# Optimization experiments

Measured on AMD Instinct MI355X. Metric: run time of the kernel, lower is better.

## Reference

```python
import jax, jax.numpy as jnp
import numpy as np
import math

B, C, H, W = 4, 256, 64, 64
G = 32  # norm_groups
EPS = 1e-5


def conv1x1(x, w, b=None):
    # x: [B,C,H,W], w: [O,C] (squeezed 1x1 kernel)
    y = jnp.einsum('bchw,oc->bohw', x, w)
    if b is not None:
        y = y + b[None, :, None, None]
    return y


def group_norm(x, gamma, beta):
    b, c, h, w = x.shape
    xg = x.reshape(b, G, c // G, h, w)
    mu = xg.mean(axis=(2, 3, 4), keepdims=True)
    var = xg.var(axis=(2, 3, 4), keepdims=True)
    xg = (xg - mu) * jax.lax.rsqrt(var + EPS)
    x = xg.reshape(b, c, h, w)
    return x * gamma[None, :, None, None] + beta[None, :, None, None]


def setup_inputs() -> dict:
    key = jax.random.key(0)
    ks = jax.random.split(key, 12)
    s = 0.02
    return {
        'x1': jax.random.normal(ks[0], (B, C, H, W), jnp.float32),
        'x2': jax.random.normal(ks[1], (B, C, H, W), jnp.float32),
        'w1': jax.random.normal(ks[2], (C, C), jnp.float32) * s,
        'b1': jnp.zeros((C,), jnp.float32),
        'w2': jax.random.normal(ks[3], (C, C), jnp.float32) * s,
        'b2': jnp.zeros((C,), jnp.float32),
        'gn_w': jnp.ones((C,), jnp.float32),
        'gn_b': jnp.zeros((C,), jnp.float32),
        'wqkv': jax.random.normal(ks[4], (3 * C, C), jnp.float32) * s,
        'wout': jax.random.normal(ks[5], (C, C), jnp.float32) * s,
        'bout': jnp.zeros((C,), jnp.float32),
        'wsk': jax.random.normal(ks[6], (C, C), jnp.float32) * s,
        'bsk': jnp.zeros((C,), jnp.float32),
    }


def reference(x1, x2, w1, b1, w2, b2, gn_w, gn_b, wqkv, wout, bout, wsk, bsk):
    x1 = conv1x1(x1, w1, b1)
    x2 = conv1x1(x2, w2, b2)

    qkv1 = conv1x1(group_norm(x1, gn_w, gn_b), wqkv)  # [B,3C,H,W]
    qkv2 = conv1x1(group_norm(x2, gn_w, gn_b), wqkv)
    q1 = qkv1[:, :C].reshape(B, C, H * W)
    k2 = qkv2[:, C:2 * C].reshape(B, C, H * W)
    v2 = qkv2[:, 2 * C:].reshape(B, C, H * W)

    # full spatial attention: [B, HW, HW]
    attn = jnp.einsum('bcq,bck->bqk', q1, k2) / math.sqrt(C)
    attn = jax.nn.softmax(attn, axis=-1)
    out = jnp.einsum('bqk,bck->bcq', attn, v2).reshape(B, C, H, W)

    out = conv1x1(out, wout, bout)
    return out + conv1x1(x1, wsk, bsk)
```

## Files before the change

kernel.cpp:

```cpp
#include <hip/hip_runtime.h>

typedef unsigned int uint;
typedef unsigned short ushort;
typedef __bf16 bf16x8 __attribute__((ext_vector_type(8)));
typedef short s16x4 __attribute__((ext_vector_type(4)));
typedef float f32x4 __attribute__((ext_vector_type(4)));

__device__ __forceinline__ ushort f2bf(float f) {
  union { float f; uint u; } c; c.f = f;
  uint u = c.u + 0x7fffu + ((c.u >> 16) & 1u);
  return (ushort)(u >> 16);
}
__device__ __forceinline__ float bflo(uint u) { union { uint u; float f; } c; c.u = u << 16; return c.f; }
__device__ __forceinline__ float bfhi(uint u) { union { uint u; float f; } c; c.u = u & 0xffff0000u; return c.f; }

__device__ __forceinline__ void gload16(const void* g, void* l) {
  __builtin_amdgcn_global_load_lds((const __attribute__((address_space(1))) void*)g,
                                   (__attribute__((address_space(3))) void*)l, 16, 0, 0);
}
__device__ __forceinline__ void mfma16(f32x4& acc, s16x4 a, s16x4 b) {
  asm("v_mfma_f32_16x16x16_bf16 %0, %1, %2, %0" : "+v"(acc) : "v"(a), "v"(b));
}
__device__ __forceinline__ float fexp2(float x) {
  float y; asm("v_exp_f32 %0, %1" : "=v"(y) : "v"(x)); return y;
}

__global__ void cast_all(const float* __restrict__ x1, const float* __restrict__ x2,
                         const float* __restrict__ w1, const float* __restrict__ w2,
                         const float* __restrict__ wqkv, const float* __restrict__ wout,
                         const float* __restrict__ wsk,
                         ushort* __restrict__ x1t, ushort* __restrict__ x2t,
                         ushort* __restrict__ w1b, ushort* __restrict__ w2b,
                         ushort* __restrict__ wqb, ushort* __restrict__ wkvb,
                         ushort* __restrict__ woutb, ushort* __restrict__ wskb) {
  const int bid = blockIdx.x, tid = threadIdx.x;
  if (bid < 8192) {
    __shared__ float t[32][33];
    const int pc = bid & 127, cc = (bid >> 7) & 7, z = bid >> 10;
    const int b = z & 3, tn = z >> 2;
    const float* x = tn ? x2 : x1;
    ushort* xt = tn ? x2t : x1t;
    const int tx = tid & 31, ty = tid >> 5;
    const float* xb = x + ((size_t)b * 256 + cc * 32) * 4096 + pc * 32;
#pragma unroll
    for (int i = 0; i < 4; ++i)
      t[ty * 4 + i][tx] = xb[(size_t)(ty * 4 + i) * 4096 + tx];
    __syncthreads();
    ushort* xtb = xt + ((size_t)b * 4096 + pc * 32) * 256 + cc * 32;
#pragma unroll
    for (int i = 0; i < 4; ++i)
      xtb[(size_t)(ty * 4 + i) * 256 + tx] = f2bf(t[tx][ty * 4 + i]);
  } else {
    const int i = (bid - 8192) * 256 + tid;
    const float QS = 0.0625f * 1.44269504088896f;
    if (i < 65536) w1b[i] = f2bf(w1[i]);
    else if (i < 131072) w2b[i - 65536] = f2bf(w2[i - 65536]);
    else if (i < 196608) wqb[i - 131072] = f2bf(wqkv[i - 131072] * QS);
    else if (i < 327680) wkvb[i - 196608] = f2bf(wqkv[i - 131072]);
    else if (i < 393216) woutb[i - 327680] = f2bf(wout[i - 327680]);
    else wskb[i - 393216] = f2bf(wsk[i - 393216]);
  }
}

__device__ __forceinline__ void g_stage_a64(const ushort* __restrict__ A,
                                            int m0, int ko, ushort* al, int w, int l) {
#pragma unroll
  for (int j = 0; j < 2; ++j) {
    int cb = (j * 4 + w) * 64;
    int chunk = cb + l;
    int row = chunk >> 3, sl = chunk & 7;
    int col = (sl * 8) ^ ((row & 7) << 3);
    gload16(A + (size_t)(m0 + row) * 256 + ko + col, al + chunk * 8);
  }
}

__device__ __forceinline__ void g_stage_b64(const ushort* __restrict__ W,
                                            int n0, int ko, ushort* bl, int w, int l) {
#pragma unroll
  for (int j = 0; j < 4; ++j) {
    int cb = (j * 4 + w) * 64;
    int chunk = cb + l;
    int row = chunk >> 3, sl = chunk & 7;
    int col = (sl * 8) ^ ((row & 7) << 3);
    gload16(W + (size_t)(n0 + row) * 256 + ko + col, bl + chunk * 8);
  }
}

__device__ __forceinline__ void g_compute64(const ushort* al, const ushort* bl,
                                            int w, int lr, int lg, f32x4 acc[4][2]) {
#pragma unroll
  for (int kk = 0; kk < 2; ++kk) {
    bf16x8 af[4], bfr[2];
#pragma unroll
    for (int m = 0; m < 4; ++m)
      af[m] = *(const bf16x8*)&al[(m * 16 + lr) * 64 + ((kk * 32 + lg * 8) ^ ((lr & 7) << 3))];
#pragma unroll
    for (int n = 0; n < 2; ++n)
      bfr[n] = *(const bf16x8*)&bl[(w * 32 + n * 16 + lr) * 64 + ((kk * 32 + lg * 8) ^ ((lr & 7) << 3))];
#pragma unroll
    for (int m = 0; m < 4; ++m)
#pragma unroll
      for (int n = 0; n < 2; ++n)
        acc[m][n] = __builtin_amdgcn_mfma_f32_16x16x32_bf16(af[m], bfr[n], acc[m][n], 0, 0, 0);
  }
}

__launch_bounds__(256)
__global__ void conv_pair(const ushort* __restrict__ x1t, const ushort* __restrict__ x2t,
                          const ushort* __restrict__ w1b, const ushort* __restrict__ w2b,
                          const float* __restrict__ b1, const float* __restrict__ b2,
                          ushort* __restrict__ y1t, ushort* __restrict__ y2t,
                          float* __restrict__ pbuf) {
  __shared__ ushort al[2][4096];
  __shared__ ushort bl[2][8192];
  const int z = blockIdx.z, b = z & 3, t = z >> 2;
  const ushort* A = (t ? x2t : x1t) + (size_t)b * 4096 * 256;
  const ushort* W = t ? w2b : w1b;
  const float* bias = t ? b2 : b1;
  ushort* out = t ? y2t : y1t;
  const int m0 = blockIdx.y * 64, n0 = blockIdx.x * 128;
  const int tid = threadIdx.x, w = tid >> 6, l = tid & 63;
  const int lr = l & 15, lg = l >> 4;
  f32x4 acc[4][2] = {};
  g_stage_a64(A, m0, 0, al[0], w, l);
  g_stage_b64(W, n0, 0, bl[0], w, l);
  __syncthreads();
  for (int s = 0; s < 4; ++s) {
    int cur = s & 1;
    if (s + 1 < 4) {
      g_stage_a64(A, m0, (s + 1) * 64, al[cur ^ 1], w, l);
      g_stage_b64(W, n0, (s + 1) * 64, bl[cur ^ 1], w, l);
    }
    g_compute64(al[cur], bl[cur], w, lr, lg, acc);
    __syncthreads();
  }
  float sg[2] = { 0.f, 0.f }, sq[2] = { 0.f, 0.f };
#pragma unroll
  for (int n = 0; n < 2; ++n) {
    int o = n0 + w * 32 + n * 16 + lr;
    float bv = bias[o];
#pragma unroll
    for (int m = 0; m < 4; ++m) {
      int p0 = m0 + m * 16 + lg * 4;
#pragma unroll
      for (int r = 0; r < 4; ++r) {
        float val = acc[m][n][r] + bv;
        out[((size_t)b * 4096 + p0 + r) * 256 + o] = f2bf(val);
        sg[n] += val; sq[n] += val * val;
      }
    }
  }
#pragma unroll
  for (int n = 0; n < 2; ++n) {
    float s1 = sg[n], s2 = sq[n];
    s1 += __shfl_xor(s1, 16); s2 += __shfl_xor(s2, 16);
    s1 += __shfl_xor(s1, 32); s2 += __shfl_xor(s2, 32);
    s1 += __shfl_xor(s1, 1);  s2 += __shfl_xor(s2, 1);
    s1 += __shfl_xor(s1, 2);  s2 += __shfl_xor(s2, 2);
    s1 += __shfl_xor(s1, 4);  s2 += __shfl_xor(s2, 4);
    if (l == 0 || l == 8) {
      int go = (n0 + w * 32 + n * 16 + (l & 8)) >> 3;
      float* dst = pbuf + (size_t)((((t * 4 + b) * 32 + go) * 64) + blockIdx.y) * 2;
      dst[0] = s1; dst[1] = s2;
    }
  }
}

__launch_bounds__(256)
__global__ void gemm_qkv(const ushort* __restrict__ y1t, const ushort* __restrict__ y2t,
                         const ushort* __restrict__ wqb, const ushort* __restrict__ wkvb,
                         const float* __restrict__ pbuf, const float* __restrict__ gn_w,
                         const float* __restrict__ gn_b,
                         ushort* __restrict__ q1t, ushort* __restrict__ k2t, ushort* __restrict__ v2) {
  __shared__ ushort al[2][4096];
  __shared__ ushort bl[2][8192];
  __shared__ float tabs[512];
  const int b = blockIdx.z, x = blockIdx.x;
  const bool isq = x < 2;
  const ushort* A = (isq ? y1t : y2t) + (size_t)b * 4096 * 256;
  const ushort* W = isq ? wqb : wkvb;
  const int n0 = isq ? x * 128 : (x - 2) * 128;
  const int m0 = blockIdx.y * 64;
  const int tid = threadIdx.x, w = tid >> 6, l = tid & 63;
  const int lr = l & 15, lg = l >> 4;

  g_stage_b64(W, n0, 0, bl[0], w, l);

  {
    const int t = isq ? 0 : 1, c = tid, g = c >> 3;
    const float* p = pbuf + (size_t)(((t * 4 + b) * 32 + g) * 64) * 2;
    float s = 0.f, ss = 0.f;
#pragma unroll 8
    for (int y = 0; y < 64; ++y) { s += p[y * 2]; ss += p[y * 2 + 1]; }
    float mu = s * (1.f / 32768.f);
    float var = ss * (1.f / 32768.f) - mu * mu;
    float rstd = rsqrtf(var + 1e-5f);
    float scale = gn_w[c] * rstd;
    tabs[2 * c] = scale;
    tabs[2 * c + 1] = gn_b[c] - mu * scale;
  }
  __syncthreads();

  int rowj[2], colj[2], ldsj[2];
#pragma unroll
  for (int j = 0; j < 2; ++j) {
    int chunk = (j * 4 + w) * 64 + l;
    int row = chunk >> 3, sl = chunk & 7;
    rowj[j] = row; colj[j] = sl * 8;
    ldsj[j] = row * 64 + ((sl * 8) ^ ((row & 7) << 3));
  }

  auto loadA = [&](int ko, uint4* av, float4 tv[2][4]) {
#pragma unroll
    for (int j = 0; j < 2; ++j) {
      av[j] = *(const uint4*)(A + (size_t)(m0 + rowj[j]) * 256 + ko + colj[j]);
      const float4* tp = (const float4*)&tabs[2 * (ko + colj[j])];
      tv[j][0] = tp[0]; tv[j][1] = tp[1]; tv[j][2] = tp[2]; tv[j][3] = tp[3];
    }
  };
  auto writeA = [&](const uint4* av, const float4 tv[2][4], ushort* al_) {
#pragma unroll
    for (int j = 0; j < 2; ++j) {
      uint rr[4] = { av[j].x, av[j].y, av[j].z, av[j].w };
      ushort o[8];
#pragma unroll
      for (int q = 0; q < 4; ++q) {
        o[q * 2]     = f2bf(bflo(rr[q]) * tv[j][q].x + tv[j][q].y);
        o[q * 2 + 1] = f2bf(bfhi(rr[q]) * tv[j][q].z + tv[j][q].w);
      }
      uint4 wv;
      wv.x = (uint)o[0] | ((uint)o[1] << 16); wv.y = (uint)o[2] | ((uint)o[3] << 16);
      wv.z = (uint)o[4] | ((uint)o[5] << 16); wv.w = (uint)o[6] | ((uint)o[7] << 16);
      *(uint4*)&al_[ldsj[j]] = wv;
    }
  };

  f32x4 acc[4][2] = {};
  {
    uint4 av[2]; float4 tv[2][4];
    loadA(0, av, tv);
    writeA(av, tv, al[0]);
  }
  __syncthreads();
  for (int s = 0; s < 4; ++s) {
    int cur = s & 1;
    uint4 av[2]; float4 tv[2][4];
    if (s + 1 < 4) {
      loadA((s + 1) * 64, av, tv);
      g_stage_b64(W, n0, (s + 1) * 64, bl[cur ^ 1], w, l);
    }
    g_compute64(al[cur], bl[cur], w, lr, lg, acc);
    if (s + 1 < 4) writeA(av, tv, al[cur ^ 1]);
    __syncthreads();
  }
#pragma unroll
  for (int n = 0; n < 2; ++n) {
    int o = n0 + w * 32 + n * 16 + lr;
#pragma unroll
    for (int m = 0; m < 4; ++m) {
      int p0 = m0 + m * 16 + lg * 4;
#pragma unroll
      for (int r = 0; r < 4; ++r) {
        float val = acc[m][n][r];
        int p = p0 + r;
        if (isq) q1t[((size_t)b * 4096 + p) * 256 + o] = f2bf(val);
        else if (o < 256) k2t[((size_t)b * 4096 + p) * 256 + o] = f2bf(val);
        else v2[((size_t)b * 256 + (o - 256)) * 4096 + p] = f2bf(val);
      }
    }
  }
}

__launch_bounds__(256)
__global__ void gemm_final(const ushort* __restrict__ op0, const ushort* __restrict__ op1,
                           const float* __restrict__ ml, const ushort* __restrict__ y1t,
                           const ushort* __restrict__ woutb, const ushort* __restrict__ wskb,
                           const float* __restrict__ bout, const float* __restrict__ bsk,
                           float* __restrict__ out) {
  __shared__ ushort smem[24576];
  ushort* al0 = smem;            ushort* al1 = smem + 4096;
  ushort* bl0 = smem + 8192;     ushort* bl1 = smem + 16384;
  const int b = blockIdx.z;
  const int m0 = blockIdx.y * 64, n0 = blockIdx.x * 128;
  const int tid = threadIdx.x, w = tid >> 6, l = tid & 63;
  const int lr = l & 15, lg = l >> 4;
  const float2* ml2 = (const float2*)ml;
  const ushort* A1 = y1t + (size_t)b * 4096 * 256;

  int rowj[2], colj[2], ldsj[2];
  float w0j[2], w1j[2];
#pragma unroll
  for (int j = 0; j < 2; ++j) {
    int chunk = (j * 4 + w) * 64 + l;
    int row = chunk >> 3, sl = chunk & 7;
    rowj[j] = row; colj[j] = sl * 8;
    ldsj[j] = row * 64 + ((sl * 8) ^ ((row & 7) << 3));
    float2 a = ml2[(size_t)b * 4096 + m0 + row];
    float2 c = ml2[(size_t)(4 + b) * 4096 + m0 + row];
    float m = fmaxf(a.x, c.x);
    float e0 = fexp2(a.x - m), e1 = fexp2(c.x - m);
    float inv = 1.f / (a.y * e0 + c.y * e1);
    w0j[j] = e0 * inv; w1j[j] = e1 * inv;
  }

  auto stageA_merge = [&](int ko, ushort* al) {
    uint4 r0[2], r1[2];
#pragma unroll
    for (int j = 0; j < 2; ++j) {
      size_t off = ((size_t)b * 4096 + m0 + rowj[j]) * 256 + ko + colj[j];
      r0[j] = *(const uint4*)(op0 + off);
      r1[j] = *(const uint4*)(op1 + off);
    }
#pragma unroll
    for (int j = 0; j < 2; ++j) {
      uint rr[4] = { r0[j].x, r0[j].y, r0[j].z, r0[j].w };
      uint ss[4] = { r1[j].x, r1[j].y, r1[j].z, r1[j].w };
      ushort o[8];
#pragma unroll
      for (int q = 0; q < 4; ++q) {
        o[q * 2]     = f2bf(bflo(rr[q]) * w0j[j] + bflo(ss[q]) * w1j[j]);
        o[q * 2 + 1] = f2bf(bfhi(rr[q]) * w0j[j] + bfhi(ss[q]) * w1j[j]);
      }
      uint4 wv;
      wv.x = (uint)o[0] | ((uint)o[1] << 16); wv.y = (uint)o[2] | ((uint)o[3] << 16);
      wv.z = (uint)o[4] | ((uint)o[5] << 16); wv.w = (uint)o[6] | ((uint)o[7] << 16);
      *(uint4*)&al[ldsj[j]] = wv;
    }
  };

  f32x4 acc[4][2] = {};
  stageA_merge(0, al0);
  g_stage_b64(woutb, n0, 0, bl0, w, l);
  __syncthreads();
  for (int s = 0; s < 8; ++s) {
    int cur = s & 1;
    if (s + 1 < 8) {
      int ko = ((s + 1) & 3) * 64;
      ushort* an = cur ? al0 : al1;
      ushort* bn = cur ? bl0 : bl1;
      if (s + 1 < 4) stageA_merge(ko, an);
      else g_stage_a64(A1, m0, ko, an, w, l);
      g_stage_b64((s + 1 >= 4) ? wskb : woutb, n0, ko, bn, w, l);
    }
    g_compute64(cur ? al1 : al0, cur ? bl1 : bl0, w, lr, lg, acc);
    __syncthreads();
  }
  float4* cl = (float4*)smem;
#pragma unroll
  for (int n = 0; n < 2; ++n) {
    int o = w * 32 + n * 16 + lr;
    float bv = bout[n0 + o] + bsk[n0 + o];
#pragma unroll
    for (int m = 0; m < 4; ++m) {
      int pf4 = m * 4 + lg;
      f32x4 v = acc[m][n];
      float4 vv; vv.x = v[0] + bv; vv.y = v[1] + bv; vv.z = v[2] + bv; vv.w = v[3] + bv;
      cl[o * 16 + (pf4 ^ (o & 15))] = vv;
    }
  }
  __syncthreads();
  float4* og = (float4*)(out + ((size_t)b * 256 + n0) * 4096 + m0);
#pragma unroll
  for (int i = 0; i < 8; ++i) {
    int o = i * 16 + (tid >> 4);
    int f4 = tid & 15;
    og[(size_t)o * 1024 + f4] = cl[o * 16 + (f4 ^ (o & 15))];
  }
}

__launch_bounds__(512, 2)
__global__ void attn(const ushort* __restrict__ Q, const ushort* __restrict__ K,
                     const ushort* __restrict__ V, ushort* __restrict__ op0,
                     ushort* __restrict__ op1, float* __restrict__ ml) {
  __shared__ ushort lds[2][40960];
  const int bid = blockIdx.x;
  const int xcd = bid & 7, r = bid >> 3;
  const int b = xcd >> 1;
  const int kh = r & 1;
  const int qt = (xcd & 1) * 16 + (r >> 1);
  const int tid = threadIdx.x;
  const int w = tid >> 6, l = tid & 63;
  const int g = w >> 2, wg = w & 3;
  const int lr = l & 15, lg = l >> 4;

  const ushort* Qb = Q + (size_t)b * 4096 * 256;
  const ushort* Kb = K + (size_t)b * 4096 * 256 + (size_t)(kh * 2048 + g * 1024) * 256;
  const ushort* Vb = V + (size_t)b * 256 * 4096 + kh * 2048 + g * 1024;

  ushort* kbuf = lds[g];
  ushort* vbuf = lds[g] + 24576;

  int kOff[4], vOff[4];
#pragma unroll
  for (int j = 0; j < 4; ++j) {
    int c = (j * 4 + wg) * 64 + l;
    int krow = c >> 5, ksl = c & 31;
    kOff[j] = krow * 256 + ((ksl * 8) ^ ((krow & 15) << 4));
    int R = c >> 2, CH = c & 3;
    int vd = R ^ ((R >> 1) & 1);
    int gch = CH ^ ((R >> 1) & 3);
    vOff[j] = vd * 4096 + gch * 8;
  }
  auto stageK = [&](int kt, ushort* dst) {
#pragma unroll
    for (int j = 0; j < 4; ++j)
      gload16(Kb + (size_t)kt * 8192 + kOff[j], dst + (j * 4 + wg) * 512);
  };
  auto stageV = [&](int kt, ushort* dst) {
#pragma unroll
    for (int j = 0; j < 4; ++j)
      gload16(Vb + (size_t)kt * 32 + vOff[j], dst + (j * 4 + wg) * 512);
  };

  bf16x8 qfA[8], qfB[8];
  {
    const ushort* qa = Qb + (size_t)(qt * 128 + wg * 32 + lr) * 256 + lg * 8;
    const ushort* qc = qa + 16 * 256;
#pragma unroll
    for (int kk = 0; kk < 8; ++kk) {
      qfA[kk] = *(const bf16x8*)(qa + kk * 32);
      qfB[kk] = *(const bf16x8*)(qc + kk * 32);
    }
  }

  stageK(0, kbuf);
  stageV(0, vbuf);
  stageK(1, kbuf + 8192);
  asm volatile("s_waitcnt vmcnt(4)" ::: "memory");
  __builtin_amdgcn_s_barrier();

  const int lrp = lr ^ ((lr >> 1) & 1);
  const int vsw = (lr >> 1) & 3;
  const int vbase0 = lrp * 32 + (((lg >> 1)) ^ vsw) * 8 + (lg & 1) * 4;
  const int vbase1 = lrp * 32 + ((2 + (lg >> 1)) ^ vsw) * 8 + (lg & 1) * 4;

  float mA = -1e30f, lsA = 0.f, mB = -1e30f, lsB = 0.f;
  f32x4 oaccA[16] = {}, oaccB[16] = {};
  int kc = 0, kn2 = 2;

  for (int kt = 0; kt < 32; ++kt) {
    const ushort* kl = kbuf + kc * 8192;
    const ushort* vl = vbuf + (kt & 1) * 8192;

    __builtin_amdgcn_s_setprio(1);
    f32x4 sA[2] = {}, sB[2] = {};
#pragma unroll
    for (int kk = 0; kk < 8; ++kk) {
#pragma unroll
      for (int n = 0; n < 2; ++n) {
        bf16x8 kv = *(const bf16x8*)&kl[(n * 16 + lr) * 256 + ((kk * 32 + lg * 8) ^ (lr << 4))];
        sA[n] = __builtin_amdgcn_mfma_f32_16x16x32_bf16(kv, qfA[kk], sA[n], 0, 0, 0);
        sB[n] = __builtin_amdgcn_mfma_f32_16x16x32_bf16(kv, qfB[kk], sB[n], 0, 0, 0);
      }
    }
    __builtin_amdgcn_s_setprio(0);

    if (kt + 1 < 32) stageV(kt + 1, vbuf + ((kt + 1) & 1) * 8192);
    if (kt + 2 < 32) stageK(kt + 2, kbuf + kn2 * 8192);

    float tmA = fmaxf(fmaxf(fmaxf(sA[0][0], sA[0][1]), fmaxf(sA[0][2], sA[0][3])),
                      fmaxf(fmaxf(sA[1][0], sA[1][1]), fmaxf(sA[1][2], sA[1][3])));
    tmA = fmaxf(tmA, __shfl_xor(tmA, 16));
    tmA = fmaxf(tmA, __shfl_xor(tmA, 32));
    float tmB = fmaxf(fmaxf(fmaxf(sB[0][0], sB[0][1]), fmaxf(sB[0][2], sB[0][3])),
                      fmaxf(fmaxf(sB[1][0], sB[1][1]), fmaxf(sB[1][2], sB[1][3])));
    tmB = fmaxf(tmB, __shfl_xor(tmB, 16));
    tmB = fmaxf(tmB, __shfl_xor(tmB, 32));

    if (__any((tmA > mA + 11.5f) || (tmB > mB + 11.5f))) {
      {
        float mn = fmaxf(mA, tmA);
        float al = fexp2(mA - mn);
        mA = mn; lsA *= al;
        float ar[4];
#pragma unroll
        for (int r2 = 0; r2 < 4; ++r2) ar[r2] = __shfl(al, lg * 4 + r2);
#pragma unroll
        for (int nf = 0; nf < 16; ++nf)
#pragma unroll
          for (int r2 = 0; r2 < 4; ++r2) oaccA[nf][r2] *= ar[r2];
      }
      {
        float mn = fmaxf(mB, tmB);
        float al = fexp2(mB - mn);
        mB = mn; lsB *= al;
        float ar[4];
#pragma unroll
        for (int r2 = 0; r2 < 4; ++r2) ar[r2] = __shfl(al, lg * 4 + r2);
#pragma unroll
        for (int nf = 0; nf < 16; ++nf)
#pragma unroll
          for (int r2 = 0; r2 < 4; ++r2) oaccB[nf][r2] *= ar[r2];
      }
    }

    uint pwA[2][2], pwB[2][2];
#pragma unroll
    for (int n = 0; n < 2; ++n) {
      float a0 = fexp2(sA[n][0] - mA), a1 = fexp2(sA[n][1] - mA);
      float a2 = fexp2(sA[n][2] - mA), a3 = fexp2(sA[n][3] - mA);
      lsA += (a0 + a1) + (a2 + a3);
      asm("v_cvt_pk_bf16_f32 %0, %1, %2" : "=v"(pwA[n][0]) : "v"(a0), "v"(a1));
      asm("v_cvt_pk_bf16_f32 %0, %1, %2" : "=v"(pwA[n][1]) : "v"(a2), "v"(a3));
      float b0 = fexp2(sB[n][0] - mB), b1 = fexp2(sB[n][1] - mB);
      float b2 = fexp2(sB[n][2] - mB), b3 = fexp2(sB[n][3] - mB);
      lsB += (b0 + b1) + (b2 + b3);
      asm("v_cvt_pk_bf16_f32 %0, %1, %2" : "=v"(pwB[n][0]) : "v"(b0), "v"(b1));
      asm("v_cvt_pk_bf16_f32 %0, %1, %2" : "=v"(pwB[n][1]) : "v"(b2), "v"(b3));
    }

    __builtin_amdgcn_s_setprio(1);
#pragma unroll
    for (int n = 0; n < 2; ++n) {
      uint2 ua; ua.x = pwA[n][0]; ua.y = pwA[n][1];
      s16x4 paA = __builtin_bit_cast(s16x4, ua);
      uint2 ub; ub.x = pwB[n][0]; ub.y = pwB[n][1];
      s16x4 paB = __builtin_bit_cast(s16x4, ub);
      const int vbase = n ? vbase1 : vbase0;
#pragma unroll
      for (int nf = 0; nf < 16; ++nf) {
        s16x4 vv = *(const s16x4*)&vl[nf * 512 + vbase];
        mfma16(oaccA[nf], paA, vv);
        mfma16(oaccB[nf], paB, vv);
      }
    }
    __builtin_amdgcn_s_setprio(0);

    if (kt < 31) {
      if (kt < 30) asm volatile("s_waitcnt vmcnt(4)" ::: "memory");
      else         asm volatile("s_waitcnt vmcnt(0)" ::: "memory");
      __builtin_amdgcn_s_barrier();
    }
    kc = (kc == 2) ? 0 : kc + 1;
    kn2 = (kn2 == 2) ? 0 : kn2 + 1;
  }

  float ra = lsA; ra += __shfl_xor(ra, 16); ra += __shfl_xor(ra, 32);
  float rb = lsB; rb += __shfl_xor(rb, 16); rb += __shfl_xor(rb, 32);

  __syncthreads();

  ushort* po = lds[0];
  float* mlm = (float*)&lds[1][0];
  float* mll = mlm + 128;

  if (g == 1) {
    if (lg == 0) {
      mlm[wg * 32 + lr] = mA;       mll[wg * 32 + lr] = ra;
      mlm[wg * 32 + 16 + lr] = mB;  mll[wg * 32 + 16 + lr] = rb;
    }
#pragma unroll
    for (int nf = 0; nf < 16; ++nf)
#pragma unroll
      for (int r2 = 0; r2 < 4; ++r2) {
        int ql = wg * 32 + lg * 4 + r2;
        po[ql * 256 + nf * 16 + lr] = f2bf(oaccA[nf][r2]);
        po[(ql + 16) * 256 + nf * 16 + lr] = f2bf(oaccB[nf][r2]);
      }
  }
  __syncthreads();
  if (g == 0) {
    float mpA = mlm[wg * 32 + lr],      lpA = mll[wg * 32 + lr];
    float mpB = mlm[wg * 32 + 16 + lr], lpB = mll[wg * 32 + 16 + lr];
    float msA = fmaxf(mA, mpA);
    float fa = fexp2(mA - msA), fb = fexp2(mpA - msA);
    float lmA = ra * fa + lpA * fb;
    float msB = fmaxf(mB, mpB);
    float fa2 = fexp2(mB - msB), fb2 = fexp2(mpB - msB);
    float lmB = rb * fa2 + lpB * fb2;
    if (lg == 0) {
      float2* ml2 = (float2*)ml;
      int qp = qt * 128 + wg * 32 + lr;
      float2 va; va.x = msA; va.y = lmA;
      ml2[((size_t)(kh * 4 + b)) * 4096 + qp] = va;
      float2 vc; vc.x = msB; vc.y = lmB;
      ml2[((size_t)(kh * 4 + b)) * 4096 + qp + 16] = vc;
    }
    float far[4], fbr[4], fa2r[4], fb2r[4];
#pragma unroll
    for (int r2 = 0; r2 < 4; ++r2) {
      far[r2] = __shfl(fa, lg * 4 + r2);   fbr[r2] = __shfl(fb, lg * 4 + r2);
      fa2r[r2] = __shfl(fa2, lg * 4 + r2); fb2r[r2] = __shfl(fb2, lg * 4 + r2);
    }
    ushort* Ob = (kh ? op1 : op0) + (size_t)b * 4096 * 256;
#pragma unroll
    for (int nf = 0; nf < 16; ++nf)
#pragma unroll
      for (int r2 = 0; r2 < 4; ++r2) {
        int ql = wg * 32 + lg * 4 + r2;
        float v1 = oaccA[nf][r2] * far[r2] + bflo((uint)po[ql * 256 + nf * 16 + lr]) * fbr[r2];
        Ob[(size_t)(qt * 128 + ql) * 256 + nf * 16 + lr] = f2bf(v1);
        float v2 = oaccB[nf][r2] * fa2r[r2] + bflo((uint)po[(ql + 16) * 256 + nf * 16 + lr]) * fb2r[r2];
        Ob[(size_t)(qt * 128 + ql + 16) * 256 + nf * 16 + lr] = f2bf(v2);
      }
  }
}

extern "C" void kernel_launch(void* const* d_in, const int* in_sizes, int n_in,
                              void* d_out, int out_size, void* d_ws, size_t ws_size,
                              hipStream_t stream) {
  const float* x1 = (const float*)d_in[0];
  const float* x2 = (const float*)d_in[1];
  const float* w1 = (const float*)d_in[2];
  const float* b1 = (const float*)d_in[3];
  const float* w2 = (const float*)d_in[4];
  const float* b2 = (const float*)d_in[5];
  const float* gn_w = (const float*)d_in[6];
  const float* gn_b = (const float*)d_in[7];
  const float* wqkv = (const float*)d_in[8];
  const float* wout = (const float*)d_in[9];
  const float* bout = (const float*)d_in[10];
  const float* wsk = (const float*)d_in[11];
  const float* bsk = (const float*)d_in[12];
  float* out = (float*)d_out;

  const size_t NB = (size_t)4 * 4096 * 256;
  ushort* x1t = (ushort*)d_ws;
  ushort* x2t = x1t + NB;
  ushort* y1t = x2t + NB;
  ushort* y2t = y1t + NB;
  ushort* g1t = y2t + NB;
  ushort* v2  = g1t + NB;
  ushort* w1b = v2 + NB;
  ushort* w2b = w1b + 65536;
  ushort* wqb = w2b + 65536;
  ushort* wkvb = wqb + 65536;
  ushort* woutb = wkvb + 131072;
  ushort* wskb = woutb + 65536;
  float* mlbuf = (float*)(wskb + 65536);
  float* pbuf  = mlbuf + 65536;

  cast_all<<<9984, 256, 0, stream>>>(x1, x2, w1, w2, wqkv, wout, wsk,
                                     x1t, x2t, w1b, w2b, wqb, wkvb, woutb, wskb);
  conv_pair<<<dim3(2, 64, 8), 256, 0, stream>>>(x1t, x2t, w1b, w2b, b1, b2, y1t, y2t, pbuf);
  gemm_qkv<<<dim3(6, 64, 4), 256, 0, stream>>>(y1t, y2t, wqb, wkvb, pbuf, gn_w, gn_b,
                                               x1t, x2t, v2);
  attn<<<256, 512, 0, stream>>>(x1t, x2t, v2, y2t, g1t, mlbuf);
  gemm_final<<<dim3(2, 64, 4), 256, 0, stream>>>(y2t, g1t, mlbuf, y1t, woutb, wskb, bout, bsk, out);
}
```

Measured before the change: 178.3 us.

## Fuse input transpose and bf16 cast into first conv GEMM

Removes the separate pass that transposed x1/x2 to channel-last bf16. conv_pair now loads fp32 activations directly, stages them through a padded LDS tile, transposes and converts them to bf16 into the swizzled A buffer. This drops a full write and reread of the transposed input tensors. The cost is a single-buffered A tile with two extra barriers per k-step, and each of the two N-blocks repeats the conversion.

```diff
diff --git a/kernel.cpp b/kernel.cpp
--- a/kernel.cpp
+++ b/kernel.cpp
@@ -25,41 +25,20 @@
   float y; asm("v_exp_f32 %0, %1" : "=v"(y) : "v"(x)); return y;
 }
 
-__global__ void cast_all(const float* __restrict__ x1, const float* __restrict__ x2,
-                         const float* __restrict__ w1, const float* __restrict__ w2,
-                         const float* __restrict__ wqkv, const float* __restrict__ wout,
-                         const float* __restrict__ wsk,
-                         ushort* __restrict__ x1t, ushort* __restrict__ x2t,
-                         ushort* __restrict__ w1b, ushort* __restrict__ w2b,
-                         ushort* __restrict__ wqb, ushort* __restrict__ wkvb,
-                         ushort* __restrict__ woutb, ushort* __restrict__ wskb) {
-  const int bid = blockIdx.x, tid = threadIdx.x;
-  if (bid < 8192) {
-    __shared__ float t[32][33];
-    const int pc = bid & 127, cc = (bid >> 7) & 7, z = bid >> 10;
-    const int b = z & 3, tn = z >> 2;
-    const float* x = tn ? x2 : x1;
-    ushort* xt = tn ? x2t : x1t;
-    const int tx = tid & 31, ty = tid >> 5;
-    const float* xb = x + ((size_t)b * 256 + cc * 32) * 4096 + pc * 32;
-#pragma unroll
-    for (int i = 0; i < 4; ++i)
-      t[ty * 4 + i][tx] = xb[(size_t)(ty * 4 + i) * 4096 + tx];
-    __syncthreads();
-    ushort* xtb = xt + ((size_t)b * 4096 + pc * 32) * 256 + cc * 32;
-#pragma unroll
-    for (int i = 0; i < 4; ++i)
-      xtb[(size_t)(ty * 4 + i) * 256 + tx] = f2bf(t[tx][ty * 4 + i]);
-  } else {
-    const int i = (bid - 8192) * 256 + tid;
-    const float QS = 0.0625f * 1.44269504088896f;
-    if (i < 65536) w1b[i] = f2bf(w1[i]);
-    else if (i < 131072) w2b[i - 65536] = f2bf(w2[i - 65536]);
-    else if (i < 196608) wqb[i - 131072] = f2bf(wqkv[i - 131072] * QS);
-    else if (i < 327680) wkvb[i - 196608] = f2bf(wqkv[i - 131072]);
-    else if (i < 393216) woutb[i - 327680] = f2bf(wout[i - 327680]);
-    else wskb[i - 393216] = f2bf(wsk[i - 393216]);
-  }
+__global__ void cast_weights(const float* __restrict__ w1, const float* __restrict__ w2,
+                             const float* __restrict__ wqkv, const float* __restrict__ wout,
+                             const float* __restrict__ wsk,
+                             ushort* __restrict__ w1b, ushort* __restrict__ w2b,
+                             ushort* __restrict__ wqb, ushort* __restrict__ wkvb,
+                             ushort* __restrict__ woutb, ushort* __restrict__ wskb) {
+  const int i = blockIdx.x * 256 + threadIdx.x;
+  const float QS = 0.0625f * 1.44269504088896f;
+  if (i < 65536) w1b[i] = f2bf(w1[i]);
+  else if (i < 131072) w2b[i - 65536] = f2bf(w2[i - 65536]);
+  else if (i < 196608) wqb[i - 131072] = f2bf(wqkv[i - 131072] * QS);
+  else if (i < 327680) wkvb[i - 196608] = f2bf(wqkv[i - 131072]);
+  else if (i < 393216) woutb[i - 327680] = f2bf(wout[i - 327680]);
+  else wskb[i - 393216] = f2bf(wsk[i - 393216]);
 }
 
 __device__ __forceinline__ void g_stage_a64(const ushort* __restrict__ A,
@@ -106,34 +85,84 @@
 }
 
 __launch_bounds__(256)
-__global__ void conv_pair(const ushort* __restrict__ x1t, const ushort* __restrict__ x2t,
+__global__ void conv_pair(const float* __restrict__ x1, const float* __restrict__ x2,
                           const ushort* __restrict__ w1b, const ushort* __restrict__ w2b,
                           const float* __restrict__ b1, const float* __restrict__ b2,
                           ushort* __restrict__ y1t, ushort* __restrict__ y2t,
                           float* __restrict__ pbuf) {
-  __shared__ ushort al[2][4096];
+  __shared__ float fb[64 * 65];
+  __shared__ ushort al[4096];
   __shared__ ushort bl[2][8192];
   const int z = blockIdx.z, b = z & 3, t = z >> 2;
-  const ushort* A = (t ? x2t : x1t) + (size_t)b * 4096 * 256;
+  const float* X = (t ? x2 : x1) + (size_t)b * 256 * 4096;
   const ushort* W = t ? w2b : w1b;
   const float* bias = t ? b2 : b1;
   ushort* out = t ? y2t : y1t;
   const int m0 = blockIdx.y * 64, n0 = blockIdx.x * 128;
   const int tid = threadIdx.x, w = tid >> 6, l = tid & 63;
   const int lr = l & 15, lg = l >> 4;
+
+  const int xrow = tid >> 2, xq = (tid & 3) * 16;
+  int ldsj[2], colj[2], rowj[2];
+#pragma unroll
+  for (int j = 0; j < 2; ++j) {
+    int chunk = (j * 4 + w) * 64 + l;
+    rowj[j] = chunk >> 3;
+    colj[j] = ((chunk & 7) * 8) ^ ((rowj[j] & 7) << 3);
+    ldsj[j] = chunk * 8;
+  }
+
+  float4 xr[4];
+  auto loadX = [&](int c0) {
+    const float* xp = X + (size_t)(c0 + xrow) * 4096 + m0 + xq;
+#pragma unroll
+    for (int i = 0; i < 4; ++i) xr[i] = *(const float4*)(xp + i * 4);
+  };
+  auto writeFB = [&]() {
+    float* fp = fb + xrow * 65 + xq;
+#pragma unroll
+    for (int i = 0; i < 4; ++i) {
+      fp[i * 4 + 0] = xr[i].x; fp[i * 4 + 1] = xr[i].y;
+      fp[i * 4 + 2] = xr[i].z; fp[i * 4 + 3] = xr[i].w;
+    }
+  };
+  auto transposeA = [&]() {
+#pragma unroll
+    for (int j = 0; j < 2; ++j) {
+      ushort o[8];
+#pragma unroll
+      for (int ii = 0; ii < 8; ++ii)
+        o[ii] = f2bf(fb[(colj[j] + ii) * 65 + rowj[j]]);
+      uint4 wv;
+      wv.x = (uint)o[0] | ((uint)o[1] << 16); wv.y = (uint)o[2] | ((uint)o[3] << 16);
+      wv.z = (uint)o[4] | ((uint)o[5] << 16); wv.w = (uint)o[6] | ((uint)o[7] << 16);
+      *(uint4*)&al[ldsj[j]] = wv;
+    }
+  };
+
   f32x4 acc[4][2] = {};
-  g_stage_a64(A, m0, 0, al[0], w, l);
+  loadX(0);
   g_stage_b64(W, n0, 0, bl[0], w, l);
-  __syncthreads();
+  writeFB();
+  __syncthreads();
+  transposeA();
+  __syncthreads();
+
   for (int s = 0; s < 4; ++s) {
     int cur = s & 1;
     if (s + 1 < 4) {
-      g_stage_a64(A, m0, (s + 1) * 64, al[cur ^ 1], w, l);
+      loadX((s + 1) * 64);
       g_stage_b64(W, n0, (s + 1) * 64, bl[cur ^ 1], w, l);
     }
-    g_compute64(al[cur], bl[cur], w, lr, lg, acc);
-    __syncthreads();
-  }
+    g_compute64(al, bl[cur], w, lr, lg, acc);
+    if (s + 1 < 4) {
+      writeFB();
+      __syncthreads();
+      transposeA();
+      __syncthreads();
+    }
+  }
+
   float sg[2] = { 0.f, 0.f }, sq[2] = { 0.f, 0.f };
 #pragma unroll
   for (int n = 0; n < 2; ++n) {
@@ -615,9 +644,9 @@
   float* out = (float*)d_out;
 
   const size_t NB = (size_t)4 * 4096 * 256;
-  ushort* x1t = (ushort*)d_ws;
-  ushort* x2t = x1t + NB;
-  ushort* y1t = x2t + NB;
+  ushort* q1t = (ushort*)d_ws;
+  ushort* k2t = q1t + NB;
+  ushort* y1t = k2t + NB;
   ushort* y2t = y1t + NB;
   ushort* g1t = y2t + NB;
   ushort* v2  = g1t + NB;
@@ -630,11 +659,11 @@
   float* mlbuf = (float*)(wskb + 65536);
   float* pbuf  = mlbuf + 65536;
 
-  cast_all<<<9984, 256, 0, stream>>>(x1, x2, w1, w2, wqkv, wout, wsk,
-                                     x1t, x2t, w1b, w2b, wqb, wkvb, woutb, wskb);
-  conv_pair<<<dim3(2, 64, 8), 256, 0, stream>>>(x1t, x2t, w1b, w2b, b1, b2, y1t, y2t, pbuf);
+  cast_weights<<<1792, 256, 0, stream>>>(w1, w2, wqkv, wout, wsk,
+                                         w1b, w2b, wqb, wkvb, woutb, wskb);
+  conv_pair<<<dim3(2, 64, 8), 256, 0, stream>>>(x1, x2, w1b, w2b, b1, b2, y1t, y2t, pbuf);
   gemm_qkv<<<dim3(6, 64, 4), 256, 0, stream>>>(y1t, y2t, wqb, wkvb, pbuf, gn_w, gn_b,
-                                               x1t, x2t, v2);
-  attn<<<256, 512, 0, stream>>>(x1t, x2t, v2, y2t, g1t, mlbuf);
+                                               q1t, k2t, v2);
+  attn<<<256, 512, 0, stream>>>(q1t, k2t, v2, y2t, g1t, mlbuf);
   gemm_final<<<dim3(2, 64, 4), 256, 0, stream>>>(y2t, g1t, mlbuf, y1t, woutb, wskb, bout, bsk, out);
 }
```

Measured after the change: 178.6 us. Within noise of the previous version (+0.1%).
